# Kernel optimization log

Hardware: AMD Instinct MI355X
Metric: run time of the kernel (lower is better)

Reference implementation:

```python
import jax, jax.numpy as jnp
import numpy as np

B, WIN, K = 8, 128, 256   # batch, window_size, n_features (nodes)
E = 2 * WIN               # embed_dim after the *2 in __init__
ALPHA = 0.2               # leaky relu negative slope


def setup_inputs() -> dict:
    key = jax.random.key(0)
    k1, k2, k3, k4 = jax.random.split(key, 4)
    x = jax.random.normal(k1, (B, WIN, K), dtype=jnp.float32)
    W_lin = jax.random.normal(k2, (E, 2 * WIN), dtype=jnp.float32) * 0.05
    b_lin = jnp.zeros((E,), dtype=jnp.float32)
    # attention vector a: [E, 1] (xavier-like small init)
    a_vec = jax.random.normal(k3, (E, 1), dtype=jnp.float32) * 0.1
    # additive bias on scores: [K, K] (zeros in torch init; small randn for generality)
    bias_mat = jax.random.normal(k4, (K, K), dtype=jnp.float32) * 0.01
    return {"x": x, "W_lin": W_lin, "b_lin": b_lin, "a_vec": a_vec, "bias_mat": bias_mat}


def reference(x, W_lin, b_lin, a_vec, bias_mat):
    v = jnp.swapaxes(x, 1, 2)
    # lin(cat(v_i, v_j)) == v_i @ W1^T + v_j @ W2^T + b, with W_lin = [W1 | W2]
    W1 = W_lin[:, :WIN]
    W2 = W_lin[:, WIN:]
    hi = v @ W1.T         # [B, K, E]
    hj = v @ W2.T         # [B, K, E]
    pre = hi[:, :, None, :] + hj[:, None, :, :] + b_lin   # [B, K, K, E]
    act = jnp.where(pre > 0, pre, ALPHA * pre)            # leaky relu
    e = (act @ a_vec)[..., 0] + bias_mat                  # [B, K, K]
    attention = jax.nn.softmax(e, axis=2)
    # dropout: eval mode (train=False) -> identity
    h = jax.nn.sigmoid(attention @ v)
    return jnp.swapaxes(h, 1, 2)
```

## Files before the change

kernel.cpp:

```cpp
#include <hip/hip_runtime.h>
#include <math.h>

namespace {
constexpr int NB   = 8;
constexpr int NWIN = 128;
constexpr int NK   = 256;
constexpr int NE   = 256;

__global__ __launch_bounds__(256) void k1_proj(
    const float* __restrict__ x, const float* __restrict__ W,
    const float* __restrict__ bl, float* __restrict__ hi,
    float* __restrict__ hjT)
{
  const int b  = blockIdx.x >> 6;
  const int e0 = (blockIdx.x & 63) << 2;
  const int i  = threadIdx.x;

  float acc1[4] = {0.f, 0.f, 0.f, 0.f};
  float acc2[4] = {0.f, 0.f, 0.f, 0.f};

  const float* xb = x + (size_t)b * NWIN * NK + i;
  const float* Wr = W + (size_t)e0 * (2 * NWIN);
#pragma unroll 8
  for (int w = 0; w < NWIN; ++w) {
    const float xv = xb[(size_t)w * NK];
#pragma unroll
    for (int k = 0; k < 4; ++k) {
      acc1[k] = fmaf(xv, Wr[k * 2 * NWIN + w], acc1[k]);
      acc2[k] = fmaf(xv, Wr[k * 2 * NWIN + NWIN + w], acc2[k]);
    }
  }

  *reinterpret_cast<float4*>(hi + ((size_t)(b * NK + i)) * NE + e0) =
      make_float4(acc1[0], acc1[1], acc1[2], acc1[3]);
#pragma unroll
  for (int k = 0; k < 4; ++k)
    hjT[((size_t)(b * NE + e0 + k)) * NK + i] = acc2[k] + bl[e0 + k];
}

__global__ __launch_bounds__(512, 4) void k2_attn(
    const float* __restrict__ x, const float* __restrict__ a_vec,
    const float* __restrict__ bias, const float* __restrict__ hi,
    const float* __restrict__ hjT, float* __restrict__ out)
{
  __shared__ __align__(16) float smA[1280];
  __shared__ __align__(16) float smB[8192];

  const int b    = blockIdx.x >> 6;
  const int i0   = (blockIdx.x & 63) << 2;
  const int t    = threadIdx.x;
  const int lane = t & 63, wave = t >> 6;

  if (t < 256) {
    ((float4*)smA)[t] =
        ((const float4*)(hi + ((size_t)(b * NK + i0)) * NE))[t];
  } else if (t < 320) {
    const float4 av = ((const float4*)a_vec)[t - 256];
    ((float4*)(smA + 1024))[t - 256] =
        make_float4(0.8f * av.x, 0.8f * av.y, 0.8f * av.z, 0.8f * av.w);
  }
  __syncthreads();

  {
    const int q = wave;
    const int j0 = lane << 2;
    float s[4][4];
#pragma unroll
    for (int ii = 0; ii < 4; ++ii)
#pragma unroll
      for (int m = 0; m < 4; ++m) s[ii][m] = 0.f;
    float aj[4] = {0.f, 0.f, 0.f, 0.f};

    const float* hjb = hjT + (size_t)b * NE * NK + j0;

#pragma unroll 2
    for (int ec = 0; ec < 8; ++ec) {
      const int e = q * 32 + ec * 4;
      float h[4][4];
#pragma unroll
      for (int k = 0; k < 4; ++k)
        *reinterpret_cast<float4*>(h[k]) =
            *reinterpret_cast<const float4*>(hjb + (size_t)(e + k) * NK);
      float a4[4];
      *reinterpret_cast<float4*>(a4) =
          *reinterpret_cast<const float4*>(smA + 1024 + e);
#pragma unroll
      for (int k = 0; k < 4; ++k)
#pragma unroll
        for (int m = 0; m < 4; ++m) aj[m] = fmaf(a4[k], h[k][m], aj[m]);
#pragma unroll
      for (int ii = 0; ii < 4; ++ii) {
        float g[4];
        *reinterpret_cast<float4*>(g) =
            *reinterpret_cast<const float4*>(smA + ii * NE + e);
#pragma unroll
        for (int k = 0; k < 4; ++k)
#pragma unroll
          for (int m = 0; m < 4; ++m)
            s[ii][m] = fmaf(a4[k], fmaxf(g[k] + h[k][m], 0.f), s[ii][m]);
      }
    }

#pragma unroll
    for (int ii = 0; ii < 4; ++ii)
      *reinterpret_cast<float4*>(&smB[(q * 4 + ii) * NK + j0]) =
          make_float4(s[ii][0] + 0.25f * aj[0], s[ii][1] + 0.25f * aj[1],
                      s[ii][2] + 0.25f * aj[2], s[ii][3] + 0.25f * aj[3]);
  }
  __syncthreads();

  if (wave < 4) {
    const int ii = wave;
    float ev[4];
    float mmax = -INFINITY;
#pragma unroll
    for (int r = 0; r < 4; ++r) {
      const int jj = lane + 64 * r;
      float v = bias[(size_t)(i0 + ii) * NK + jj];
#pragma unroll
      for (int qq = 0; qq < 8; ++qq) v += smB[(qq * 4 + ii) * NK + jj];
      ev[r] = v;
      mmax = fmaxf(mmax, v);
    }
#pragma unroll
    for (int o = 32; o; o >>= 1) mmax = fmaxf(mmax, __shfl_xor(mmax, o));
    float ssum = 0.f;
#pragma unroll
    for (int r = 0; r < 4; ++r) { ev[r] = __expf(ev[r] - mmax); ssum += ev[r]; }
#pragma unroll
    for (int o = 32; o; o >>= 1) ssum += __shfl_xor(ssum, o);
    const float inv = 1.f / ssum;
#pragma unroll
    for (int r = 0; r < 4; ++r) smA[ii * NE + lane + 64 * r] = ev[r] * inv;
  }
  __syncthreads();

  {
    const int wv = t >> 2, jq = t & 3;
    float s0 = 0.f, s1 = 0.f, s2 = 0.f, s3 = 0.f;
    const float* xr = x + (size_t)b * NWIN * NK + (size_t)wv * NK;
#pragma unroll 4
    for (int jc = 0; jc < 16; ++jc) {
      const int j = jc * 16 + jq * 4;
      const float4 xv = *reinterpret_cast<const float4*>(&xr[j]);
      const float4 a0 = *reinterpret_cast<const float4*>(&smA[0 * NE + j]);
      const float4 a1 = *reinterpret_cast<const float4*>(&smA[1 * NE + j]);
      const float4 a2 = *reinterpret_cast<const float4*>(&smA[2 * NE + j]);
      const float4 a3 = *reinterpret_cast<const float4*>(&smA[3 * NE + j]);
      s0 = fmaf(a0.x, xv.x, s0); s0 = fmaf(a0.y, xv.y, s0);
      s0 = fmaf(a0.z, xv.z, s0); s0 = fmaf(a0.w, xv.w, s0);
      s1 = fmaf(a1.x, xv.x, s1); s1 = fmaf(a1.y, xv.y, s1);
      s1 = fmaf(a1.z, xv.z, s1); s1 = fmaf(a1.w, xv.w, s1);
      s2 = fmaf(a2.x, xv.x, s2); s2 = fmaf(a2.y, xv.y, s2);
      s2 = fmaf(a2.z, xv.z, s2); s2 = fmaf(a2.w, xv.w, s2);
      s3 = fmaf(a3.x, xv.x, s3); s3 = fmaf(a3.y, xv.y, s3);
      s3 = fmaf(a3.z, xv.z, s3); s3 = fmaf(a3.w, xv.w, s3);
    }
#pragma unroll
    for (int o = 1; o <= 2; o <<= 1) {
      s0 += __shfl_xor(s0, o);
      s1 += __shfl_xor(s1, o);
      s2 += __shfl_xor(s2, o);
      s3 += __shfl_xor(s3, o);
    }
    if (jq == 0) {
      float4 o4;
      o4.x = 1.f / (1.f + __expf(-s0));
      o4.y = 1.f / (1.f + __expf(-s1));
      o4.z = 1.f / (1.f + __expf(-s2));
      o4.w = 1.f / (1.f + __expf(-s3));
      *reinterpret_cast<float4*>(out + ((size_t)(b * NWIN + wv)) * NK + i0) =
          o4;
    }
  }
}

}

extern "C" void kernel_launch(void* const* d_in, const int* in_sizes, int n_in,
                              void* d_out, int out_size, void* d_ws,
                              size_t ws_size, hipStream_t stream)
{
  const float* x    = (const float*)d_in[0];
  const float* Wlin = (const float*)d_in[1];
  const float* blin = (const float*)d_in[2];
  const float* avec = (const float*)d_in[3];
  const float* bias = (const float*)d_in[4];
  float* out = (float*)d_out;

  float* hi  = (float*)d_ws;
  float* hjT = hi + (size_t)NB * NK * NE;

  k1_proj<<<NB * (NE / 4), 256, 0, stream>>>(x, Wlin, blin, hi, hjT);
  k2_attn<<<NB * (NK / 4), 512, 0, stream>>>(x, avec, bias, hi, hjT, out);
}
```

Baseline: 34.28 us.

## Fuse projection and attention kernels via cooperative grid sync

Merges the projection and attention kernels into one cooperative kernel that uses a grid-wide barrier between the phases. This removes the second kernel launch and the gap between launches. The projection phase is reworked so each 512-thread block computes the same 4 embedding columns, with each thread handling 2 columns. If the cooperative launch fails it falls back to two separate launches. The grid barrier adds its own synchronisation cost, and the fused kernel must keep all 512 blocks resident at once.

```diff
diff --git a/kernel.cpp b/kernel.cpp
--- a/kernel.cpp
+++ b/kernel.cpp
@@ -1,5 +1,8 @@
 #include <hip/hip_runtime.h>
+#include <hip/hip_cooperative_groups.h>
 #include <math.h>
+
+namespace cg = cooperative_groups;
 
 namespace {
 constexpr int NB   = 8;
@@ -7,48 +10,40 @@
 constexpr int NK   = 256;
 constexpr int NE   = 256;
 
-__global__ __launch_bounds__(256) void k1_proj(
+__device__ __forceinline__ void proj_phase(
     const float* __restrict__ x, const float* __restrict__ W,
     const float* __restrict__ bl, float* __restrict__ hi,
-    float* __restrict__ hjT)
-{
-  const int b  = blockIdx.x >> 6;
-  const int e0 = (blockIdx.x & 63) << 2;
-  const int i  = threadIdx.x;
-
-  float acc1[4] = {0.f, 0.f, 0.f, 0.f};
-  float acc2[4] = {0.f, 0.f, 0.f, 0.f};
-
+    float* __restrict__ hjT, int bid, int t)
+{
+  const int b  = bid >> 6;
+  const int e0 = ((bid & 63) << 2) + ((t >> 8) << 1);
+  const int i  = t & 255;
+
+  float a1x = 0.f, a1y = 0.f, a2x = 0.f, a2y = 0.f;
   const float* xb = x + (size_t)b * NWIN * NK + i;
   const float* Wr = W + (size_t)e0 * (2 * NWIN);
 #pragma unroll 8
   for (int w = 0; w < NWIN; ++w) {
     const float xv = xb[(size_t)w * NK];
-#pragma unroll
-    for (int k = 0; k < 4; ++k) {
-      acc1[k] = fmaf(xv, Wr[k * 2 * NWIN + w], acc1[k]);
-      acc2[k] = fmaf(xv, Wr[k * 2 * NWIN + NWIN + w], acc2[k]);
-    }
-  }
-
-  *reinterpret_cast<float4*>(hi + ((size_t)(b * NK + i)) * NE + e0) =
-      make_float4(acc1[0], acc1[1], acc1[2], acc1[3]);
-#pragma unroll
-  for (int k = 0; k < 4; ++k)
-    hjT[((size_t)(b * NE + e0 + k)) * NK + i] = acc2[k] + bl[e0 + k];
-}
-
-__global__ __launch_bounds__(512, 4) void k2_attn(
+    a1x = fmaf(xv, Wr[w], a1x);
+    a2x = fmaf(xv, Wr[NWIN + w], a2x);
+    a1y = fmaf(xv, Wr[2 * NWIN + w], a1y);
+    a2y = fmaf(xv, Wr[3 * NWIN + w], a2y);
+  }
+  *reinterpret_cast<float2*>(hi + ((size_t)(b * NK + i)) * NE + e0) =
+      make_float2(a1x, a1y);
+  hjT[((size_t)(b * NE + e0)) * NK + i]     = a2x + bl[e0];
+  hjT[((size_t)(b * NE + e0 + 1)) * NK + i] = a2y + bl[e0 + 1];
+}
+
+__device__ __forceinline__ void attn_phase(
     const float* __restrict__ x, const float* __restrict__ a_vec,
     const float* __restrict__ bias, const float* __restrict__ hi,
-    const float* __restrict__ hjT, float* __restrict__ out)
-{
-  __shared__ __align__(16) float smA[1280];
-  __shared__ __align__(16) float smB[8192];
-
-  const int b    = blockIdx.x >> 6;
-  const int i0   = (blockIdx.x & 63) << 2;
-  const int t    = threadIdx.x;
+    const float* __restrict__ hjT, float* __restrict__ out,
+    int bid, int t, float* smA, float* smB)
+{
+  const int b    = bid >> 6;
+  const int i0   = (bid & 63) << 2;
   const int lane = t & 63, wave = t >> 6;
 
   if (t < 256) {
@@ -175,6 +170,41 @@
   }
 }
 
+__global__ __launch_bounds__(512, 4) void fused(
+    const float* __restrict__ x, const float* __restrict__ W,
+    const float* __restrict__ bl, const float* __restrict__ a_vec,
+    const float* __restrict__ bias, float* __restrict__ hi,
+    float* __restrict__ hjT, float* __restrict__ out)
+{
+  __shared__ __align__(16) float smA[1280];
+  __shared__ __align__(16) float smB[8192];
+
+  const int bid = blockIdx.x;
+  const int t   = threadIdx.x;
+
+  proj_phase(x, W, bl, hi, hjT, bid, t);
+  cg::this_grid().sync();
+  attn_phase(x, a_vec, bias, hi, hjT, out, bid, t, smA, smB);
+}
+
+__global__ __launch_bounds__(512) void k1_proj(
+    const float* __restrict__ x, const float* __restrict__ W,
+    const float* __restrict__ bl, float* __restrict__ hi,
+    float* __restrict__ hjT)
+{
+  proj_phase(x, W, bl, hi, hjT, blockIdx.x, threadIdx.x);
+}
+
+__global__ __launch_bounds__(512, 4) void k2_attn(
+    const float* __restrict__ x, const float* __restrict__ a_vec,
+    const float* __restrict__ bias, const float* __restrict__ hi,
+    const float* __restrict__ hjT, float* __restrict__ out)
+{
+  __shared__ __align__(16) float smA[1280];
+  __shared__ __align__(16) float smB[8192];
+  attn_phase(x, a_vec, bias, hi, hjT, out, blockIdx.x, threadIdx.x, smA, smB);
+}
+
 }
 
 extern "C" void kernel_launch(void* const* d_in, const int* in_sizes, int n_in,
@@ -191,6 +221,12 @@
   float* hi  = (float*)d_ws;
   float* hjT = hi + (size_t)NB * NK * NE;
 
-  k1_proj<<<NB * (NE / 4), 256, 0, stream>>>(x, Wlin, blin, hi, hjT);
-  k2_attn<<<NB * (NK / 4), 512, 0, stream>>>(x, avec, bias, hi, hjT, out);
-}
+  void* args[] = {(void*)&x, (void*)&Wlin, (void*)&blin, (void*)&avec,
+                  (void*)&bias, (void*)&hi, (void*)&hjT, (void*)&out};
+  hipError_t err = hipLaunchCooperativeKernel(
+      (const void*)&fused, dim3(NB * (NK / 4)), dim3(512), args, 0, stream);
+  if (err != hipSuccess) {
+    k1_proj<<<NB * (NE / 4), 512, 0, stream>>>(x, Wlin, blin, hi, hjT);
+    k2_attn<<<NB * (NK / 4), 512, 0, stream>>>(x, avec, bias, hi, hjT, out);
+  }
+}
```

Measured after the change: 121.4 us. 3.54x slower.
